# Kernel optimization log

Measured on AMD Instinct MI355X. Metric: run time of the kernel, lower is better.

The kernel has to match this reference:

```python
import jax, jax.numpy as jnp
import numpy as np

NR, NL, K, TOPK, C, B = 4096, 16384, 8, 10, 16, 4
W_OCC, W_MDN, W_INT = 0.2, 1.0, 0.1
LOG2PI = float(np.log(2.0 * np.pi))


def setup_inputs() -> dict:
    key = jax.random.key(0)
    ks = jax.random.split(key, 12)
    radar_indices = jnp.concatenate([
        jax.random.randint(ks[0], (NR, 1), 0, B),
        jax.random.randint(ks[1], (NR, 1), 0, 41),
        jax.random.randint(ks[2], (NR, 2), 0, 176),
    ], axis=1).astype(jnp.int32)
    lidar_indices = jnp.concatenate([
        jax.random.randint(ks[3], (NL, 1), 0, B),
        jax.random.randint(ks[4], (NL, 1), 0, 41),
        jax.random.randint(ks[5], (NL, 2), 0, 176),
    ], axis=1).astype(jnp.int32)
    return {
        'mu_off': jax.random.normal(ks[6], (NR, K, 3)) * 2.0,
        'log_sig_off': jax.random.normal(ks[7], (NR, K, 3)) * 0.3,
        'mu_int': jax.random.normal(ks[8], (NR, K, 1)),
        'occ_logit': jax.random.normal(ks[9], (NR, K, 1)),
        'mix_logit': jax.random.normal(ks[10], (NR, K, 1)),
        'lidar_features': jax.random.normal(ks[11], (NL, C)),
        'radar_indices': radar_indices,
        'lidar_indices': lidar_indices,
        'gt_topk': TOPK,
    }


def _match(radar_indices, lidar_indices, topk):
    # per-batch top-k nearest lidar voxels for each radar voxel (vectorized:
    # dense masked distance matrix replaces the per-batch python loop)
    rb, lb = radar_indices[:, 0], lidar_indices[:, 0]
    rpos = radar_indices[:, 1:].astype(jnp.float32)  # (Nr,3) zyx
    lpos = lidar_indices[:, 1:].astype(jnp.float32)  # (Nl,3)
    d2 = ((rpos * rpos).sum(-1)[:, None] + (lpos * lpos).sum(-1)[None, :]
          - 2.0 * (rpos @ lpos.T))  # (Nr,Nl) squared dist, same order as cdist
    same = rb[:, None] == lb[None, :]
    d2 = jnp.where(same, d2, jnp.inf)  # cross-batch pairs excluded
    _, nn_idx = jax.lax.top_k(-d2, topk)  # (Nr,topk) smallest distances
    matched = same.any(axis=1)  # (Nr,)
    offs_zyx = (lidar_indices[nn_idx, 1:]
                - radar_indices[:, None, 1:]).astype(jnp.float32)  # (Nr,topk,3)
    offs_zyx = jnp.where(matched[:, None, None], offs_zyx, 0.0)
    return matched, nn_idx, offs_zyx


def reference(mu_off, log_sig_off, mu_int, occ_logit, mix_logit,
              lidar_features, radar_indices, lidar_indices, gt_topk):
    matched, nn_idx, offs_zyx = _match(radar_indices, lidar_indices, gt_topk)
    gt_feat = jnp.where(matched[:, None, None], lidar_features[nn_idx], 0.0)  # (Nr,T,C)
    y = offs_zyx[..., ::-1]  # flip zyx -> xyz, (Nr,T,3)

    # occupancy BCE-with-logits against matched mask
    occ_any = occ_logit[..., 0].max(axis=1)  # (Nr,)
    tgt = matched.astype(occ_any.dtype)
    occ_loss = (tgt * jax.nn.softplus(-occ_any)
                + (1.0 - tgt) * jax.nn.softplus(occ_any)).mean()

    # MDN log-prob: (Nr,T,K) mixture components
    log_pi = jax.nn.log_softmax(mix_logit[..., 0], axis=1)  # (Nr,K)
    mu_ = mu_off[:, None, :, :]       # (Nr,1,K,3)
    ls_ = log_sig_off[:, None, :, :]
    sigma2 = jnp.exp(2.0 * ls_) + 1e-12
    y_ = y[:, :, None, :]             # (Nr,T,1,3)
    logN = -0.5 * (((y_ - mu_) ** 2) / sigma2 + 2.0 * ls_ + LOG2PI).sum(-1)  # (Nr,T,K)
    log_post = logN + log_pi[:, None, :]
    logp = jax.nn.logsumexp(log_post, axis=-1)  # (Nr,T)

    # masked means emulate boolean-index-then-mean over matched rows
    m = matched.astype(jnp.float32)
    cnt = m.sum()
    T = logp.shape[1]
    mdn_nll = -(logp * m[:, None]).sum() / (cnt * T)

    # intensity loss (C % 4 == 0 path)
    gt_int = gt_feat.reshape(gt_feat.shape[0], gt_feat.shape[1], C // 4, 4)[..., 3].mean(axis=2)  # (Nr,T)
    r = jax.nn.softmax(log_post, axis=-1)  # (Nr,T,K) responsibilities
    term = r * jnp.abs(mu_int[:, None, :, 0] - gt_int[:, :, None])  # (Nr,T,K)
    int_loss = (term * m[:, None, None]).sum() / (cnt * T * r.shape[-1])

    return W_OCC * occ_loss + W_MDN * mdn_nll + W_INT * int_loss
```

## Files before the change

### kernel.cpp

```cpp
#include <hip/hip_runtime.h>
#include <cstdint>

#define NRAD 4096
#define NLID 16384
#define KMIX 8
#define TOPK 10
#define CF   16
#define LOG2PI 1.8378770664093453f

static constexpr unsigned INF_D2 = 62851u;

__device__ __forceinline__ void insert_key(unsigned (&t)[TOPK], unsigned key) {
#pragma unroll
    for (int i = TOPK - 1; i >= 1; --i) {
        unsigned hi = key > t[i - 1] ? key : t[i - 1];
        t[i] = hi < t[i] ? hi : t[i];
    }
    t[0] = key < t[0] ? key : t[0];
}

__device__ __forceinline__ void merge10(unsigned (&t)[TOPK], int lane,
                                        unsigned& mine, unsigned& first, unsigned& tenth) {
#pragma unroll
    for (int r = 0; r < TOPK; ++r) {
        unsigned v = t[0];
#pragma unroll
        for (int off = 32; off >= 1; off >>= 1) {
            unsigned o = __shfl_xor(v, off, 64);
            v = o < v ? o : v;
        }
        if (t[0] == v) {
#pragma unroll
            for (int i = 0; i < TOPK - 1; ++i) t[i] = t[i + 1];
            t[TOPK - 1] = 0xFFFFFFFFu;
        }
        if (lane == r) mine = v;
        if (r == 0) first = v;
        if (r == TOPK - 1) tenth = v;
    }
}

__device__ __forceinline__ float waveReduceSum(float v) {
#pragma unroll
    for (int off = 32; off >= 1; off >>= 1) v += __shfl_down(v, off, 64);
    return v;
}

__global__ __launch_bounds__(1024) void prep_kernel(
        const int* __restrict__ lidar_indices,
        unsigned* __restrict__ packed_full,
        uint2* __restrict__ compacted,
        int* __restrict__ meta,
        float* __restrict__ accum) {
    __shared__ int hist[4];
    __shared__ int cursor[4];
    int tid = threadIdx.x;
    int lane = tid & 63;
    if (tid < 4) { hist[tid] = 0; accum[tid] = 0.f; }
    __syncthreads();

    int pb[16]; unsigned pp[16];
    int local[4] = {0, 0, 0, 0};
#pragma unroll
    for (int it = 0; it < 16; ++it) {
        int i = it * 1024 + tid;
        int4 li = ((const int4*)lidar_indices)[i];
        int b = li.x;
        unsigned pos = ((unsigned)li.y << 16) | ((unsigned)li.z << 8) | (unsigned)li.w;
        packed_full[i] = ((unsigned)b << 22) | pos;
        pb[it] = b; pp[it] = pos;
#pragma unroll
        for (int b2 = 0; b2 < 4; ++b2)
            local[b2] += (int)__popcll(__ballot(b == b2));
    }
    if (lane == 0) {
#pragma unroll
        for (int b2 = 0; b2 < 4; ++b2) atomicAdd(&hist[b2], local[b2]);
    }
    __syncthreads();
    if (tid == 0) {
        int b0 = 0;
#pragma unroll
        for (int b2 = 0; b2 < 4; ++b2) {
            meta[b2] = hist[b2];
            meta[4 + b2] = b0;
            cursor[b2] = b0;
            b0 = (b0 + hist[b2] + 1) & ~1;
        }
    }
    __syncthreads();
#pragma unroll
    for (int it = 0; it < 16; ++it) {
        int i = it * 1024 + tid;
        int b = pb[it];
#pragma unroll
        for (int b2 = 0; b2 < 4; ++b2) {
            unsigned long long mask = __ballot(b == b2);
            if (b == b2) {
                int leader = __ffsll((unsigned long long)mask) - 1;
                int off = (int)__popcll(mask & ((1ull << lane) - 1ull));
                int s = 0;
                if (lane == leader) s = atomicAdd(&cursor[b2], (int)__popcll(mask));
                s = __shfl(s, leader, 64);
                compacted[s + off] = make_uint2(pp[it], (unsigned)i);
            }
        }
    }
}

__global__ __launch_bounds__(256) void topk_kernel(
        const uint2* __restrict__ compacted,
        const unsigned* __restrict__ packed_full,
        const int* __restrict__ meta,
        const int* __restrict__ radar_indices,
        int* __restrict__ nn_out, int* __restrict__ matched_out) {
    int lane = threadIdx.x & 63;
    int row  = blockIdx.x * 4 + (threadIdx.x >> 6);
    int4 ri = ((const int4*)radar_indices)[row];
    int rb = ri.x, rz = ri.y, ry = ri.z, rx = ri.w;
    int c_cnt  = meta[rb];
    int c_base = meta[4 + rb];

    unsigned t[TOPK];
#pragma unroll
    for (int i = 0; i < TOPK; ++i) t[i] = 0xFFFFFFFFu;

    const uint4* src = (const uint4*)(compacted + c_base);
    int iters = (c_cnt + 127) >> 7;
    for (int it = 0; it < iters; ++it) {
        uint4 q = src[it * 64 + lane];
        int c0 = (it * 64 + lane) * 2;
        {
            int z = (int)((q.x >> 16) & 63u), y = (int)((q.x >> 8) & 255u), x = (int)(q.x & 255u);
            int dz = z - rz, dy = y - ry, dx = x - rx;
            unsigned d2 = (unsigned)(dz * dz + dy * dy + dx * dx);
            unsigned key = (c0 < c_cnt) ? ((d2 << 14) | q.y) : 0xFFFFFFFFu;
            insert_key(t, key);
        }
        {
            int z = (int)((q.z >> 16) & 63u), y = (int)((q.z >> 8) & 255u), x = (int)(q.z & 255u);
            int dz = z - rz, dy = y - ry, dx = x - rx;
            unsigned d2 = (unsigned)(dz * dz + dy * dy + dx * dx);
            unsigned key = (c0 + 1 < c_cnt) ? ((d2 << 14) | q.w) : 0xFFFFFFFFu;
            insert_key(t, key);
        }
    }

    unsigned mine = 0, first = 0, tenth = 0;
    merge10(t, lane, mine, first, tenth);
    bool matched = true;

    if (tenth == 0xFFFFFFFFu) {
#pragma unroll
        for (int i = 0; i < TOPK; ++i) t[i] = 0xFFFFFFFFu;
        for (int it = 0; it < NLID / 256; ++it) {
            uint4 p4 = ((const uint4*)packed_full)[it * 64 + lane];
            unsigned base = it * 256 + lane * 4;
            unsigned ps[4] = {p4.x, p4.y, p4.z, p4.w};
#pragma unroll
            for (int j = 0; j < 4; ++j) {
                unsigned p = ps[j];
                int b  = (int)(p >> 22);
                int dz = (int)((p >> 16) & 63u)  - rz;
                int dy = (int)((p >> 8)  & 255u) - ry;
                int dx = (int)(p & 255u)         - rx;
                unsigned d2 = (unsigned)(dz * dz + dy * dy + dx * dx);
                unsigned hi = (b == rb) ? d2 : INF_D2;
                insert_key(t, (hi << 14) | (base + j));
            }
        }
        merge10(t, lane, mine, first, tenth);
        matched = first < (INF_D2 << 14);
    }

    if (lane < TOPK) nn_out[row * TOPK + lane] = (int)(mine & 0x3FFFu);
    if (lane == 0)   matched_out[row] = matched ? 1 : 0;
}

__global__ __launch_bounds__(256) void mdn_kernel(
        const float* __restrict__ mu_off, const float* __restrict__ log_sig_off,
        const float* __restrict__ mu_int, const float* __restrict__ occ_logit,
        const float* __restrict__ mix_logit, const float* __restrict__ lidar_features,
        const int* __restrict__ radar_indices, const int* __restrict__ lidar_indices,
        const int* __restrict__ nn, const int* __restrict__ matched,
        float* __restrict__ accum) {
    int gid = blockIdx.x * 256 + threadIdx.x;
    int n  = gid / TOPK;
    int tt = gid - n * TOPK;
    int m  = matched[n];
    float mf = (float)m;
    int nni = nn[gid];

    int4 ri = ((const int4*)radar_indices)[n];
    int4 li = ((const int4*)lidar_indices)[nni];
    float y0 = mf * (float)(li.w - ri.w);
    float y1 = mf * (float)(li.z - ri.z);
    float y2 = mf * (float)(li.y - ri.y);

    float mix[KMIX];
    float mmax = -1e30f;
#pragma unroll
    for (int k = 0; k < KMIX; ++k) {
        mix[k] = mix_logit[n * KMIX + k];
        mmax = fmaxf(mmax, mix[k]);
    }
    float msum = 0.f;
#pragma unroll
    for (int k = 0; k < KMIX; ++k) msum += expf(mix[k] - mmax);
    float logZ = mmax + logf(msum);

    float lpost[KMIX];
    float pmax = -1e30f;
#pragma unroll
    for (int k = 0; k < KMIX; ++k) {
        int bidx = (n * KMIX + k) * 3;
        float mu0 = mu_off[bidx + 0], mu1 = mu_off[bidx + 1], mu2 = mu_off[bidx + 2];
        float l0 = log_sig_off[bidx + 0], l1 = log_sig_off[bidx + 1], l2 = log_sig_off[bidx + 2];
        float s0 = expf(2.f * l0) + 1e-12f;
        float s1 = expf(2.f * l1) + 1e-12f;
        float s2 = expf(2.f * l2) + 1e-12f;
        float d0 = y0 - mu0, d1 = y1 - mu1, d2v = y2 - mu2;
        float q = d0 * d0 / s0 + d1 * d1 / s1 + d2v * d2v / s2
                + 2.f * (l0 + l1 + l2) + 3.f * LOG2PI;
        lpost[k] = -0.5f * q + (mix[k] - logZ);
        pmax = fmaxf(pmax, lpost[k]);
    }
    float ex[KMIX];
    float se = 0.f;
#pragma unroll
    for (int k = 0; k < KMIX; ++k) { ex[k] = expf(lpost[k] - pmax); se += ex[k]; }
    float logp = pmax + logf(se);

    float gt = 0.f;
    if (m) {
        const float* lf = lidar_features + nni * CF;
        gt = 0.25f * (lf[3] + lf[7] + lf[11] + lf[15]);
    }
    float inv_se = 1.f / se;
    float isum = 0.f;
#pragma unroll
    for (int k = 0; k < KMIX; ++k)
        isum += ex[k] * inv_se * fabsf(mu_int[n * KMIX + k] - gt);

    float lp = mf * logp;
    float ip = mf * isum;
    float oc = 0.f, mc = 0.f;
    if (tt == 0) {
        float oa = -1e30f;
#pragma unroll
        for (int k = 0; k < KMIX; ++k) oa = fmaxf(oa, occ_logit[n * KMIX + k]);
        float soft_abs = log1pf(expf(-fabsf(oa)));
        float sp_neg = soft_abs + fmaxf(-oa, 0.f);
        float sp_pos = soft_abs + fmaxf(oa, 0.f);
        oc = mf * sp_neg + (1.f - mf) * sp_pos;
        mc = mf;
    }

    lp = waveReduceSum(lp); ip = waveReduceSum(ip);
    oc = waveReduceSum(oc); mc = waveReduceSum(mc);
    __shared__ float sA[4], sB[4], sC[4], sD[4];
    int wid = threadIdx.x >> 6, lane = threadIdx.x & 63;
    if (lane == 0) { sA[wid] = lp; sB[wid] = ip; sC[wid] = oc; sD[wid] = mc; }
    __syncthreads();
    if (threadIdx.x == 0) {
        atomicAdd(&accum[0], sA[0] + sA[1] + sA[2] + sA[3]);
        atomicAdd(&accum[1], sB[0] + sB[1] + sB[2] + sB[3]);
        atomicAdd(&accum[2], sC[0] + sC[1] + sC[2] + sC[3]);
        atomicAdd(&accum[3], sD[0] + sD[1] + sD[2] + sD[3]);
    }
}

__global__ void final_kernel(const float* __restrict__ accum, float* __restrict__ out) {
    if (threadIdx.x == 0) {
        float cnt = accum[3];
        float occ_loss = accum[2] / (float)NRAD;
        float mdn_nll  = -accum[0] / (cnt * (float)TOPK);
        float int_loss = accum[1] / (cnt * (float)TOPK * (float)KMIX);
        out[0] = 0.2f * occ_loss + mdn_nll + 0.1f * int_loss;
    }
}

extern "C" void kernel_launch(void* const* d_in, const int* in_sizes, int n_in,
                              void* d_out, int out_size, void* d_ws, size_t ws_size,
                              hipStream_t stream) {
    const float* mu_off         = (const float*)d_in[0];
    const float* log_sig_off    = (const float*)d_in[1];
    const float* mu_int         = (const float*)d_in[2];
    const float* occ_logit      = (const float*)d_in[3];
    const float* mix_logit      = (const float*)d_in[4];
    const float* lidar_features = (const float*)d_in[5];
    const int*   radar_indices  = (const int*)d_in[6];
    const int*   lidar_indices  = (const int*)d_in[7];
    float* out = (float*)d_out;

    char* ws = (char*)d_ws;
    unsigned* packed_full = (unsigned*)(ws + 0);
    uint2*    compacted   = (uint2*)(ws + 65536);
    int*      meta        = (int*)(ws + 204800);
    float*    accum       = (float*)(ws + 204864);
    int*      nn          = (int*)(ws + 208896);
    int*      matched     = (int*)(ws + 372736);

    hipLaunchKernelGGL(prep_kernel, dim3(1), dim3(1024), 0, stream,
                       lidar_indices, packed_full, compacted, meta, accum);
    hipLaunchKernelGGL(topk_kernel, dim3(NRAD / 4), dim3(256), 0, stream,
                       compacted, packed_full, meta, radar_indices, nn, matched);
    hipLaunchKernelGGL(mdn_kernel, dim3(NRAD * TOPK / 256), dim3(256), 0, stream,
                       mu_off, log_sig_off, mu_int, occ_logit, mix_logit,
                       lidar_features, radar_indices, lidar_indices,
                       nn, matched, accum);
    hipLaunchKernelGGL(final_kernel, dim3(1), dim3(64), 0, stream, accum, out);
}
```

Before: 126.3 us.

## Parallelize lidar compaction across blocks and fold final reduction into MDN kernel

The single-block prep kernel becomes a multi-block kernel. Each block uses global atomic cursors and writes into fixed per-batch regions of size NLID, so the prefix scan is no longer needed. The top-k loop now prefetches the next tile and skips insertion when a key cannot enter the current top-10. The separate final kernel is replaced by a last-block-done counter inside the MDN kernel, and a memset zeroes the counters. This removes a serial single-CU stage and one launch, at the cost of non-deterministic compaction order, which could in principle change how distance ties are broken.

Result: faster. 121.8 us (-3.6%).

```diff
diff --git a/kernel.cpp b/kernel.cpp
--- a/kernel.cpp
+++ b/kernel.cpp
@@ -46,64 +46,27 @@
     return v;
 }
 
-__global__ __launch_bounds__(1024) void prep_kernel(
+__global__ __launch_bounds__(256) void prep_kernel(
         const int* __restrict__ lidar_indices,
         unsigned* __restrict__ packed_full,
         uint2* __restrict__ compacted,
-        int* __restrict__ meta,
-        float* __restrict__ accum) {
-    __shared__ int hist[4];
-    __shared__ int cursor[4];
-    int tid = threadIdx.x;
-    int lane = tid & 63;
-    if (tid < 4) { hist[tid] = 0; accum[tid] = 0.f; }
-    __syncthreads();
-
-    int pb[16]; unsigned pp[16];
-    int local[4] = {0, 0, 0, 0};
-#pragma unroll
-    for (int it = 0; it < 16; ++it) {
-        int i = it * 1024 + tid;
-        int4 li = ((const int4*)lidar_indices)[i];
-        int b = li.x;
-        unsigned pos = ((unsigned)li.y << 16) | ((unsigned)li.z << 8) | (unsigned)li.w;
-        packed_full[i] = ((unsigned)b << 22) | pos;
-        pb[it] = b; pp[it] = pos;
-#pragma unroll
-        for (int b2 = 0; b2 < 4; ++b2)
-            local[b2] += (int)__popcll(__ballot(b == b2));
-    }
-    if (lane == 0) {
-#pragma unroll
-        for (int b2 = 0; b2 < 4; ++b2) atomicAdd(&hist[b2], local[b2]);
-    }
-    __syncthreads();
-    if (tid == 0) {
-        int b0 = 0;
-#pragma unroll
-        for (int b2 = 0; b2 < 4; ++b2) {
-            meta[b2] = hist[b2];
-            meta[4 + b2] = b0;
-            cursor[b2] = b0;
-            b0 = (b0 + hist[b2] + 1) & ~1;
-        }
-    }
-    __syncthreads();
-#pragma unroll
-    for (int it = 0; it < 16; ++it) {
-        int i = it * 1024 + tid;
-        int b = pb[it];
-#pragma unroll
-        for (int b2 = 0; b2 < 4; ++b2) {
-            unsigned long long mask = __ballot(b == b2);
-            if (b == b2) {
-                int leader = __ffsll((unsigned long long)mask) - 1;
-                int off = (int)__popcll(mask & ((1ull << lane) - 1ull));
-                int s = 0;
-                if (lane == leader) s = atomicAdd(&cursor[b2], (int)__popcll(mask));
-                s = __shfl(s, leader, 64);
-                compacted[s + off] = make_uint2(pp[it], (unsigned)i);
-            }
+        int* __restrict__ cursor) {
+    int i = blockIdx.x * 256 + threadIdx.x;
+    int lane = threadIdx.x & 63;
+    int4 li = ((const int4*)lidar_indices)[i];
+    int b = li.x;
+    unsigned pos = ((unsigned)li.y << 16) | ((unsigned)li.z << 8) | (unsigned)li.w;
+    packed_full[i] = ((unsigned)b << 22) | pos;
+#pragma unroll
+    for (int b2 = 0; b2 < 4; ++b2) {
+        unsigned long long mask = __ballot(b == b2);
+        if (b == b2) {
+            int leader = __ffsll(mask) - 1;
+            int off = (int)__popcll(mask & ((1ull << lane) - 1ull));
+            int s = 0;
+            if (lane == leader) s = atomicAdd(&cursor[b2], (int)__popcll(mask));
+            s = __shfl(s, leader, 64);
+            compacted[b2 * NLID + s + off] = make_uint2(pos, (unsigned)i);
         }
     }
 }
@@ -111,39 +74,43 @@
 __global__ __launch_bounds__(256) void topk_kernel(
         const uint2* __restrict__ compacted,
         const unsigned* __restrict__ packed_full,
-        const int* __restrict__ meta,
+        const int* __restrict__ cursor,
         const int* __restrict__ radar_indices,
         int* __restrict__ nn_out, int* __restrict__ matched_out) {
     int lane = threadIdx.x & 63;
     int row  = blockIdx.x * 4 + (threadIdx.x >> 6);
     int4 ri = ((const int4*)radar_indices)[row];
     int rb = ri.x, rz = ri.y, ry = ri.z, rx = ri.w;
-    int c_cnt  = meta[rb];
-    int c_base = meta[4 + rb];
+    int c_cnt = cursor[rb];
 
     unsigned t[TOPK];
 #pragma unroll
     for (int i = 0; i < TOPK; ++i) t[i] = 0xFFFFFFFFu;
 
-    const uint4* src = (const uint4*)(compacted + c_base);
+    const uint4* src = (const uint4*)(compacted + rb * NLID);
     int iters = (c_cnt + 127) >> 7;
+    uint4 q = src[lane];
     for (int it = 0; it < iters; ++it) {
-        uint4 q = src[it * 64 + lane];
+        uint4 qn = q;
+        if (it + 1 < iters) qn = src[(it + 1) * 64 + lane];
         int c0 = (it * 64 + lane) * 2;
         {
-            int z = (int)((q.x >> 16) & 63u), y = (int)((q.x >> 8) & 255u), x = (int)(q.x & 255u);
-            int dz = z - rz, dy = y - ry, dx = x - rx;
+            int dz = (int)((q.x >> 16) & 63u)  - rz;
+            int dy = (int)((q.x >> 8)  & 255u) - ry;
+            int dx = (int)(q.x & 255u)         - rx;
             unsigned d2 = (unsigned)(dz * dz + dy * dy + dx * dx);
             unsigned key = (c0 < c_cnt) ? ((d2 << 14) | q.y) : 0xFFFFFFFFu;
-            insert_key(t, key);
+            if (key < t[TOPK - 1]) insert_key(t, key);
         }
         {
-            int z = (int)((q.z >> 16) & 63u), y = (int)((q.z >> 8) & 255u), x = (int)(q.z & 255u);
-            int dz = z - rz, dy = y - ry, dx = x - rx;
+            int dz = (int)((q.z >> 16) & 63u)  - rz;
+            int dy = (int)((q.z >> 8)  & 255u) - ry;
+            int dx = (int)(q.z & 255u)         - rx;
             unsigned d2 = (unsigned)(dz * dz + dy * dy + dx * dx);
             unsigned key = (c0 + 1 < c_cnt) ? ((d2 << 14) | q.w) : 0xFFFFFFFFu;
-            insert_key(t, key);
-        }
+            if (key < t[TOPK - 1]) insert_key(t, key);
+        }
+        q = qn;
     }
 
     unsigned mine = 0, first = 0, tenth = 0;
@@ -183,7 +150,9 @@
         const float* __restrict__ mix_logit, const float* __restrict__ lidar_features,
         const int* __restrict__ radar_indices, const int* __restrict__ lidar_indices,
         const int* __restrict__ nn, const int* __restrict__ matched,
-        float* __restrict__ accum) {
+        float* __restrict__ accum,
+        unsigned* __restrict__ dctr,
+        float* __restrict__ out) {
     int gid = blockIdx.x * 256 + threadIdx.x;
     int n  = gid / TOPK;
     int tt = gid - n * TOPK;
@@ -250,9 +219,7 @@
 #pragma unroll
         for (int k = 0; k < KMIX; ++k) oa = fmaxf(oa, occ_logit[n * KMIX + k]);
         float soft_abs = log1pf(expf(-fabsf(oa)));
-        float sp_neg = soft_abs + fmaxf(-oa, 0.f);
-        float sp_pos = soft_abs + fmaxf(oa, 0.f);
-        oc = mf * sp_neg + (1.f - mf) * sp_pos;
+        oc = mf * (soft_abs + fmaxf(-oa, 0.f)) + (1.f - mf) * (soft_abs + fmaxf(oa, 0.f));
         mc = mf;
     }
 
@@ -267,16 +234,19 @@
         atomicAdd(&accum[1], sB[0] + sB[1] + sB[2] + sB[3]);
         atomicAdd(&accum[2], sC[0] + sC[1] + sC[2] + sC[3]);
         atomicAdd(&accum[3], sD[0] + sD[1] + sD[2] + sD[3]);
-    }
-}
-
-__global__ void final_kernel(const float* __restrict__ accum, float* __restrict__ out) {
-    if (threadIdx.x == 0) {
-        float cnt = accum[3];
-        float occ_loss = accum[2] / (float)NRAD;
-        float mdn_nll  = -accum[0] / (cnt * (float)TOPK);
-        float int_loss = accum[1] / (cnt * (float)TOPK * (float)KMIX);
-        out[0] = 0.2f * occ_loss + mdn_nll + 0.1f * int_loss;
+        __threadfence();
+        unsigned done = atomicAdd(dctr, 1u);
+        if (done == gridDim.x - 1) {
+            __threadfence();
+            float a = __hip_atomic_load(&accum[0], __ATOMIC_RELAXED, __HIP_MEMORY_SCOPE_AGENT);
+            float b = __hip_atomic_load(&accum[1], __ATOMIC_RELAXED, __HIP_MEMORY_SCOPE_AGENT);
+            float c = __hip_atomic_load(&accum[2], __ATOMIC_RELAXED, __HIP_MEMORY_SCOPE_AGENT);
+            float d = __hip_atomic_load(&accum[3], __ATOMIC_RELAXED, __HIP_MEMORY_SCOPE_AGENT);
+            float occ_loss = c / (float)NRAD;
+            float mdn_nll  = -a / (d * (float)TOPK);
+            float int_loss = b / (d * (float)TOPK * (float)KMIX);
+            out[0] = 0.2f * occ_loss + mdn_nll + 0.1f * int_loss;
+        }
     }
 }
 
@@ -296,18 +266,20 @@
     char* ws = (char*)d_ws;
     unsigned* packed_full = (unsigned*)(ws + 0);
     uint2*    compacted   = (uint2*)(ws + 65536);
-    int*      meta        = (int*)(ws + 204800);
-    float*    accum       = (float*)(ws + 204864);
-    int*      nn          = (int*)(ws + 208896);
-    int*      matched     = (int*)(ws + 372736);
-
-    hipLaunchKernelGGL(prep_kernel, dim3(1), dim3(1024), 0, stream,
-                       lidar_indices, packed_full, compacted, meta, accum);
+    int*      cursor      = (int*)(ws + 589824);
+    float*    accum       = (float*)(ws + 589840);
+    unsigned* dctr        = (unsigned*)(ws + 589856);
+    int*      nn          = (int*)(ws + 589888);
+    int*      matched     = (int*)(ws + 753728);
+
+    hipMemsetAsync(ws + 589824, 0, 64, stream);
+
+    hipLaunchKernelGGL(prep_kernel, dim3(NLID / 256), dim3(256), 0, stream,
+                       lidar_indices, packed_full, compacted, cursor);
     hipLaunchKernelGGL(topk_kernel, dim3(NRAD / 4), dim3(256), 0, stream,
-                       compacted, packed_full, meta, radar_indices, nn, matched);
+                       compacted, packed_full, cursor, radar_indices, nn, matched);
     hipLaunchKernelGGL(mdn_kernel, dim3(NRAD * TOPK / 256), dim3(256), 0, stream,
                        mu_off, log_sig_off, mu_int, occ_logit, mix_logit,
                        lidar_features, radar_indices, lidar_indices,
-                       nn, matched, accum);
-    hipLaunchKernelGGL(final_kernel, dim3(1), dim3(64), 0, stream, accum, out);
-}
+                       nn, matched, accum, dctr, out);
+}
```
